# Optimization experiments

Hardware: AMD Instinct MI355X
Metric: run time of the kernel (lower is better)

## Reference

```python
import jax, jax.numpy as jnp
import numpy as np

D_MODEL = 1024
NUM_HEADS = 16
GROUP_SIZE = 4
NUM_GROUPS = NUM_HEADS // GROUP_SIZE  # 4
D_K = D_MODEL // NUM_HEADS            # 64
THETA = 10000.0
WINDOW = 512


def _rope(x, positions):
    # x: (..., t, d) with d even; interleaved-pair rotation, freq_i = theta^{-i/(d/2)}
    d = x.shape[-1]
    half = d // 2
    inv_freq = THETA ** (-jnp.arange(half, dtype=x.dtype) / half)          # (half,)
    ang = positions.astype(x.dtype)[:, None] * inv_freq[None, :]           # (t, half)
    cos, sin = jnp.cos(ang), jnp.sin(ang)
    x1, x2 = x[..., 0::2], x[..., 1::2]
    r1 = x1 * cos - x2 * sin
    r2 = x1 * sin + x2 * cos
    return jnp.stack([r1, r2], axis=-1).reshape(x.shape)


def setup_inputs() -> dict:
    key = jax.random.key(0)
    k1, k2, k3, k4, k5 = jax.random.split(key, 5)
    b, t = 2, 2048
    scale = 1.0 / np.sqrt(D_MODEL)
    return {
        "x": jax.random.normal(k1, (b, t, D_MODEL), dtype=jnp.float32),
        "WQ": jax.random.normal(k2, (D_MODEL, D_MODEL), dtype=jnp.float32) * scale,
        "WK": jax.random.normal(k3, (NUM_GROUPS * D_K, D_MODEL), dtype=jnp.float32) * scale,
        "WV": jax.random.normal(k4, (NUM_GROUPS * D_K, D_MODEL), dtype=jnp.float32) * scale,
        "WO": jax.random.normal(k5, (D_MODEL, D_MODEL), dtype=jnp.float32) * scale,
        "token_positions": jnp.arange(t, dtype=jnp.int32),
    }


def reference(x, WQ, WK, WV, WO, token_positions):
    b, t, _ = x.shape
    g, s, d = NUM_GROUPS, GROUP_SIZE, D_K
    # projections (Linear: y = x @ W^T, no bias)
    q = (x @ WQ.T).reshape(b, t, g, s, d).transpose(0, 2, 3, 1, 4)  # b g s t d
    k = (x @ WK.T).reshape(b, t, g, d).transpose(0, 2, 1, 3)        # b g t d
    v = (x @ WV.T).reshape(b, t, g, d).transpose(0, 2, 1, 3)        # b g t d
    q = _rope(q, token_positions)
    k = _rope(k, token_positions)
    # scores: kv heads shared across the s query heads of each group
    scores = jnp.einsum('bgsqd,bgkd->bgsqk', q, k) / jnp.sqrt(jnp.asarray(d, x.dtype))
    i = jnp.arange(t)[:, None]
    j = jnp.arange(t)[None, :]
    allowed = (i >= j) & (i - j <= WINDOW)  # causal sliding window
    scores = jnp.where(allowed, scores, -jnp.inf)
    probs = jax.nn.softmax(scores, axis=-1)
    out = jnp.einsum('bgsqk,bgkd->bgsqd', probs, v)                 # b g s t d
    out = out.transpose(0, 3, 1, 2, 4).reshape(b, t, D_MODEL)       # b t (g s d)
    return out @ WO.T
```

## Files before the change

### kernel.cpp

```cpp
#include <hip/hip_runtime.h>
#include <hip/hip_bf16.h>

typedef __bf16 bf16;
typedef __bf16 bf16x4 __attribute__((ext_vector_type(4)));
typedef __bf16 bf16x8 __attribute__((ext_vector_type(8)));
typedef float  floatx4 __attribute__((ext_vector_type(4)));

#define D_MODEL   1024
#define NUM_HEADS 16
#define NUM_GROUPS 4
#define DK        64
#define SEQ_T     2048
#define BATCH     2
#define M_ROWS    (BATCH*SEQ_T)
#define WINDOW    512
#define KV_DIM    (NUM_GROUPS*DK)
#define N_QKV     (D_MODEL + 2*KV_DIM)
#define QSCALE    0.1803368801111204f
#define FREQ_C    0.4152410118609203f

#define GLDS16(g, l)                                                          \
    __builtin_amdgcn_global_load_lds(                                         \
        (const __attribute__((address_space(1))) void*)(g),                   \
        (__attribute__((address_space(3))) void*)(l), 16, 0, 0)

__global__ __launch_bounds__(256)
void convert_all(const float* s0, bf16* d0, int c0,
                 const float* s1, bf16* d1, int c1,
                 const float* s2, bf16* d2, int c2,
                 const float* s3, bf16* d3, int c3,
                 const float* s4, bf16* d4, int c4)
{
    int id = blockIdx.x * 256 + threadIdx.x;
    const float* src; bf16* dst;
    if      (id < c0)         { src = s0; dst = d0; }
    else if ((id -= c0) < c1) { src = s1; dst = d1; }
    else if ((id -= c1) < c2) { src = s2; dst = d2; }
    else if ((id -= c2) < c3) { src = s3; dst = d3; }
    else if ((id -= c3) < c4) { src = s4; dst = d4; }
    else return;
    int i = id * 8;
    const float* s = src + i;
    float4 a = *(const float4*)s;
    float4 b = *(const float4*)(s + 4);
    bf16x8 v;
    v[0] = (bf16)a.x; v[1] = (bf16)a.y; v[2] = (bf16)a.z; v[3] = (bf16)a.w;
    v[4] = (bf16)b.x; v[5] = (bf16)b.y; v[6] = (bf16)b.z; v[7] = (bf16)b.w;
    *(bf16x8*)&dst[i] = v;
}

__global__ __launch_bounds__(256, 6)
void gemm_t64(const bf16* __restrict__ A, const bf16* __restrict__ W, int K,
              bf16* __restrict__ Cq, bf16* __restrict__ Ck, bf16* __restrict__ Vt,
              float* __restrict__ Co, const int* __restrict__ pos, int mode)
{
    __shared__ bf16 As0[64 * 32], As1[64 * 32];
    __shared__ bf16 Bs0[64 * 32], Bs1[64 * 32];

    const int tid  = threadIdx.x;
    const int wave = tid >> 6;
    const int lane = tid & 63;
    const int lr   = lane & 15;
    const int quad = lane >> 4;
    const int m0 = blockIdx.y * 64;
    const int n0 = blockIdx.x * 64;
    const int wm = (wave >> 1) * 32;
    const int wn = (wave & 1) * 32;

    const int srow = (lane >> 2);
    const int scol = (lane & 3) * 8;
    const bf16* Ap = &A[(size_t)(m0 + wave * 16 + srow) * K + scol];
    const bf16* Wp = &W[(size_t)(n0 + wave * 16 + srow) * K + scol];
    bf16* As0d = &As0[wave * 512];
    bf16* As1d = &As1[wave * 512];
    bf16* Bs0d = &Bs0[wave * 512];
    bf16* Bs1d = &Bs1[wave * 512];

    floatx4 acc[2][2];
#pragma unroll
    for (int i = 0; i < 2; i++)
#pragma unroll
        for (int j = 0; j < 2; j++) acc[i][j] = (floatx4)(0.0f);

    for (int k0 = 0; k0 < K; k0 += 64) {
        __syncthreads();
        GLDS16(Ap + k0,      As0d);
        GLDS16(Ap + k0 + 32, As1d);
        GLDS16(Wp + k0,      Bs0d);
        GLDS16(Wp + k0 + 32, Bs1d);
        __syncthreads();

        bf16x8 a0[2], a1[2], b0[2], b1[2];
#pragma unroll
        for (int mi = 0; mi < 2; mi++) {
            a0[mi] = *(const bf16x8*)&As0[(wm + mi * 16 + lr) * 32 + quad * 8];
            a1[mi] = *(const bf16x8*)&As1[(wm + mi * 16 + lr) * 32 + quad * 8];
        }
#pragma unroll
        for (int ni = 0; ni < 2; ni++) {
            b0[ni] = *(const bf16x8*)&Bs0[(wn + ni * 16 + lr) * 32 + quad * 8];
            b1[ni] = *(const bf16x8*)&Bs1[(wn + ni * 16 + lr) * 32 + quad * 8];
        }

#pragma unroll
        for (int mi = 0; mi < 2; mi++)
#pragma unroll
            for (int ni = 0; ni < 2; ni++) {
                acc[mi][ni] = __builtin_amdgcn_mfma_f32_16x16x32_bf16(
                    a0[mi], b0[ni], acc[mi][ni], 0, 0, 0);
                acc[mi][ni] = __builtin_amdgcn_mfma_f32_16x16x32_bf16(
                    a1[mi], b1[ni], acc[mi][ni], 0, 0, 0);
            }
    }

    if (mode == 0) {
        if (n0 >= D_MODEL + KV_DIM) {
            const int g  = (n0 - (D_MODEL + KV_DIM)) >> 6;
            const int b  = m0 >> 11;
            const int bg = b * 4 + g;
#pragma unroll
            for (int mi = 0; mi < 2; mi++) {
#pragma unroll
                for (int ni = 0; ni < 2; ni++) {
                    int d  = wn + ni * 16 + lr;
                    int t0 = (m0 & (SEQ_T - 1)) + wm + mi * 16 + quad * 4;
                    bf16x4 v;
#pragma unroll
                    for (int r = 0; r < 4; r++) v[r] = (bf16)acc[mi][ni][r];
                    *(bf16x4*)&Vt[((size_t)(bg * 64 + d)) * SEQ_T + t0] = v;
                }
            }
        } else {
            bf16* out; int ld, coff; float sc;
            if (n0 < D_MODEL) { out = Cq; ld = D_MODEL; coff = n0; sc = QSCALE; }
            else              { out = Ck; ld = KV_DIM;  coff = n0 - D_MODEL; sc = 1.0f; }
            float inv[2];
            float sgn = (lr & 1) ? 1.0f : -1.0f;
#pragma unroll
            for (int ni = 0; ni < 2; ni++) {
                int ip = (wn + ni * 16 + lr) >> 1;
                inv[ni] = exp2f(-(float)ip * FREQ_C);
            }
#pragma unroll
            for (int mi = 0; mi < 2; mi++) {
#pragma unroll
                for (int r = 0; r < 4; r++) {
                    int row = m0 + wm + mi * 16 + quad * 4 + r;
                    float p = (float)pos[row & (SEQ_T - 1)];
#pragma unroll
                    for (int ni = 0; ni < 2; ni++) {
                        float v  = acc[mi][ni][r];
                        float vp = __shfl_xor(v, 1);
                        float ang = p * inv[ni];
                        float ss, cc;
                        __sincosf(ang, &ss, &cc);
                        v = v * cc + vp * ss * sgn;
                        out[(size_t)row * ld + coff + wn + ni * 16 + lr] = (bf16)(v * sc);
                    }
                }
            }
        }
    } else {
#pragma unroll
        for (int mi = 0; mi < 2; mi++)
#pragma unroll
            for (int ni = 0; ni < 2; ni++)
#pragma unroll
                for (int r = 0; r < 4; r++) {
                    int row = m0 + wm + mi * 16 + quad * 4 + r;
                    int col = n0 + wn + ni * 16 + lr;
                    Co[(size_t)row * D_MODEL + col] = acc[mi][ni][r];
                }
    }
}

__global__ __launch_bounds__(256)
void attn_mfma(const bf16* __restrict__ Q, const bf16* __restrict__ K,
               const bf16* __restrict__ Vt_g, bf16* __restrict__ AO)
{
    const int ST = 72;
    __shared__ bf16 Ks[64 * ST];
    __shared__ bf16 Vt[80 * ST];
    __shared__ bf16 Ps[4 * 32 * ST];

    const int tid  = threadIdx.x;
    const int wave = tid >> 6;
    const int lane = tid & 63;
    const int lr   = lane & 15;
    const int quad = lane >> 4;
    const int bg = blockIdx.y;
    const int b = bg >> 2, g = bg & 3;
    const int h = g * 4 + wave;
    const int q0 = blockIdx.x * 32;

    bf16x8 qf[2][2];
#pragma unroll
    for (int mi = 0; mi < 2; mi++)
#pragma unroll
        for (int ks = 0; ks < 2; ks++)
            qf[mi][ks] = *(const bf16x8*)
                &Q[((size_t)(b * SEQ_T + q0 + mi * 16 + lr)) * D_MODEL
                   + h * 64 + ks * 32 + quad * 8];

    for (int i = tid; i < 15 * ST; i += 256) Vt[65 * ST + i] = (bf16)0.0f;
    if (tid < ST) Vt[64 * ST + tid] = (bf16)(tid < 64 ? 1.0f : 0.0f);

    bf16* Pw = &Ps[wave * 32 * ST];

    floatx4 o[2][5];
#pragma unroll
    for (int mi = 0; mi < 2; mi++)
#pragma unroll
        for (int nt = 0; nt < 5; nt++) o[mi][nt] = (floatx4)(0.0f);

    const int t0   = (q0 >= WINDOW) ? ((q0 - WINDOW) & ~63) : 0;
    const int last = q0 & ~63;

    for (int j0 = t0; j0 <= last; j0 += 64) {
        const bool mC = (j0 == last);
        const bool mW = (q0 >= WINDOW) && (j0 == t0);
        __syncthreads();
#pragma unroll
        for (int i = 0; i < 2; i++) {
            int c = tid + i * 256;
            int row = c >> 3, col8 = (c & 7) * 8;
            *(bf16x8*)&Ks[row * ST + col8] =
                *(const bf16x8*)&K[((size_t)(b * SEQ_T + j0 + row)) * KV_DIM + g * 64 + col8];
            *(bf16x8*)&Vt[row * ST + col8] =
                *(const bf16x8*)&Vt_g[((size_t)(bg * 64 + row)) * SEQ_T + j0 + col8];
        }
        __syncthreads();

        floatx4 s[2][4];
#pragma unroll
        for (int mi = 0; mi < 2; mi++)
#pragma unroll
            for (int nt = 0; nt < 4; nt++) s[mi][nt] = (floatx4)(0.0f);
#pragma unroll
        for (int ks = 0; ks < 2; ks++) {
#pragma unroll
            for (int nt = 0; nt < 4; nt++) {
                bf16x8 kf = *(const bf16x8*)&Ks[(nt * 16 + lr) * ST + ks * 32 + quad * 8];
                s[0][nt] = __builtin_amdgcn_mfma_f32_16x16x32_bf16(qf[0][ks], kf, s[0][nt], 0, 0, 0);
                s[1][nt] = __builtin_amdgcn_mfma_f32_16x16x32_bf16(qf[1][ks], kf, s[1][nt], 0, 0, 0);
            }
        }

        if (mC) {
#pragma unroll
            for (int mi = 0; mi < 2; mi++)
#pragma unroll
                for (int nt = 0; nt < 4; nt++) {
                    int key = j0 + nt * 16 + lr;
#pragma unroll
                    for (int r = 0; r < 4; r++) {
                        int qi_ = q0 + mi * 16 + quad * 4 + r;
                        s[mi][nt][r] = (key <= qi_) ? s[mi][nt][r] : -1e30f;
                    }
                }
        } else if (mW) {
#pragma unroll
            for (int mi = 0; mi < 2; mi++)
#pragma unroll
                for (int nt = 0; nt < 4; nt++) {
                    int key = j0 + nt * 16 + lr;
#pragma unroll
                    for (int r = 0; r < 4; r++) {
                        int qi_ = q0 + mi * 16 + quad * 4 + r;
                        s[mi][nt][r] = (qi_ - key <= WINDOW) ? s[mi][nt][r] : -1e30f;
                    }
                }
        }

#pragma unroll
        for (int mi = 0; mi < 2; mi++)
#pragma unroll
            for (int nt = 0; nt < 4; nt++)
#pragma unroll
                for (int r = 0; r < 4; r++)
                    Pw[(mi * 16 + quad * 4 + r) * ST + nt * 16 + lr] =
                        (bf16)exp2f(s[mi][nt][r]);

        __asm__ volatile("s_waitcnt lgkmcnt(0)" ::: "memory");

#pragma unroll
        for (int ks = 0; ks < 2; ks++) {
            bf16x8 pf0 = *(const bf16x8*)&Pw[(0 + lr) * ST + ks * 32 + quad * 8];
            bf16x8 pf1 = *(const bf16x8*)&Pw[(16 + lr) * ST + ks * 32 + quad * 8];
#pragma unroll
            for (int nt = 0; nt < 5; nt++) {
                bf16x8 vf = *(const bf16x8*)&Vt[(nt * 16 + lr) * ST + ks * 32 + quad * 8];
                o[0][nt] = __builtin_amdgcn_mfma_f32_16x16x32_bf16(pf0, vf, o[0][nt], 0, 0, 0);
                o[1][nt] = __builtin_amdgcn_mfma_f32_16x16x32_bf16(pf1, vf, o[1][nt], 0, 0, 0);
            }
        }
    }

#pragma unroll
    for (int mi = 0; mi < 2; mi++)
#pragma unroll
        for (int r = 0; r < 4; r++) {
            float l = __shfl(o[mi][4][r], lane & 48);
            float invl = 1.0f / l;
            int row = q0 + mi * 16 + quad * 4 + r;
#pragma unroll
            for (int nt = 0; nt < 4; nt++)
                AO[((size_t)(b * SEQ_T + row)) * D_MODEL + h * 64 + nt * 16 + lr] =
                    (bf16)(o[mi][nt][r] * invl);
        }
}

extern "C" void kernel_launch(void* const* d_in, const int* in_sizes, int n_in,
                              void* d_out, int out_size, void* d_ws, size_t ws_size,
                              hipStream_t stream)
{
    const float* x  = (const float*)d_in[0];
    const float* WQ = (const float*)d_in[1];
    const float* WK = (const float*)d_in[2];
    const float* WV = (const float*)d_in[3];
    const float* WO = (const float*)d_in[4];
    const int*  pos = (const int*)d_in[5];

    char* ws   = (char*)d_ws;
    bf16* Qw   = (bf16*)ws;
    bf16* Kw   = (bf16*)(ws + (size_t) 8 * 1024 * 1024);
    bf16* Vt_g = (bf16*)(ws + (size_t)10 * 1024 * 1024);
    bf16* xb   = (bf16*)(ws + (size_t)12 * 1024 * 1024);
    bf16* AO   = xb;
    bf16* Wqkv = (bf16*)(ws + (size_t)20 * 1024 * 1024);
    bf16* WOb  = (bf16*)(ws + (size_t)23 * 1024 * 1024);

    const int cx = (M_ROWS * D_MODEL) / 8;
    const int cq = (D_MODEL * D_MODEL) / 8;
    const int ck = (KV_DIM * D_MODEL) / 8;
    const int ctot = cx + cq + 2 * ck + cq;
    convert_all<<<ctot / 256, 256, 0, stream>>>(
        x, xb, cx,
        WQ, Wqkv, cq,
        WK, Wqkv + (size_t)D_MODEL * D_MODEL, ck,
        WV, Wqkv + (size_t)(D_MODEL + KV_DIM) * D_MODEL, ck,
        WO, WOb, cq);

    gemm_t64<<<dim3(N_QKV / 64, M_ROWS / 64), 256, 0, stream>>>(
        x ? xb : xb, Wqkv, D_MODEL, Qw, Kw, Vt_g, nullptr, pos, 0);

    attn_mfma<<<dim3(SEQ_T / 32, BATCH * NUM_GROUPS), 256, 0, stream>>>(
        Qw, Kw, Vt_g, AO);

    gemm_t64<<<dim3(D_MODEL / 64, M_ROWS / 64), 256, 0, stream>>>(
        AO, WOb, D_MODEL, nullptr, nullptr, nullptr, (float*)d_out, pos, 1);
}
```

Baseline: 150.1 us.

## Fuse all stages into one persistent kernel with grid-wide barriers

Replaces the four launches (convert, QKV GEMM, attention, output GEMM) with one persistent kernel of 512 blocks that runs each stage in turn and separates them with a software grid barrier built on atomics. Each block handles 3 QKV tiles, one attention tile and 2 output-projection tiles, and shared memory is reused across stages through a union. The aim is to remove launch gaps and tail effects between kernels. In exchange it depends on all 512 blocks being co-resident for the spin barrier, adds a memset, and lowers the launch-bounds occupancy hint to 3 blocks per CU, which could hurt latency hiding in the GEMMs.

Result: slower. 329.8 us (+119.8%).

```diff
diff --git a/kernel.cpp b/kernel.cpp
--- a/kernel.cpp
+++ b/kernel.cpp
@@ -18,76 +18,60 @@
 #define N_QKV     (D_MODEL + 2*KV_DIM)
 #define QSCALE    0.1803368801111204f
 #define FREQ_C    0.4152410118609203f
+#define GRID_B    512
 
 #define GLDS16(g, l)                                                          \
     __builtin_amdgcn_global_load_lds(                                         \
         (const __attribute__((address_space(1))) void*)(g),                   \
         (__attribute__((address_space(3))) void*)(l), 16, 0, 0)
 
-__global__ __launch_bounds__(256)
-void convert_all(const float* s0, bf16* d0, int c0,
-                 const float* s1, bf16* d1, int c1,
-                 const float* s2, bf16* d2, int c2,
-                 const float* s3, bf16* d3, int c3,
-                 const float* s4, bf16* d4, int c4)
+__device__ __forceinline__ void gbar(int* cnt, int* gen, int nb)
 {
-    int id = blockIdx.x * 256 + threadIdx.x;
-    const float* src; bf16* dst;
-    if      (id < c0)         { src = s0; dst = d0; }
-    else if ((id -= c0) < c1) { src = s1; dst = d1; }
-    else if ((id -= c1) < c2) { src = s2; dst = d2; }
-    else if ((id -= c2) < c3) { src = s3; dst = d3; }
-    else if ((id -= c3) < c4) { src = s4; dst = d4; }
-    else return;
-    int i = id * 8;
-    const float* s = src + i;
-    float4 a = *(const float4*)s;
-    float4 b = *(const float4*)(s + 4);
-    bf16x8 v;
-    v[0] = (bf16)a.x; v[1] = (bf16)a.y; v[2] = (bf16)a.z; v[3] = (bf16)a.w;
-    v[4] = (bf16)b.x; v[5] = (bf16)b.y; v[6] = (bf16)b.z; v[7] = (bf16)b.w;
-    *(bf16x8*)&dst[i] = v;
+    __syncthreads();
+    if (threadIdx.x == 0) {
+        __threadfence();
+        int g = atomicAdd(gen, 0);
+        int a = atomicAdd(cnt, 1);
+        if (a == nb - 1) {
+            atomicSub(cnt, nb);
+            __threadfence();
+            atomicAdd(gen, 1);
+        } else {
+            while (atomicAdd(gen, 0) == g) __builtin_amdgcn_s_sleep(2);
+        }
+        __threadfence();
+    }
+    __syncthreads();
 }
 
-__global__ __launch_bounds__(256, 6)
-void gemm_t64(const bf16* __restrict__ A, const bf16* __restrict__ W, int K,
-              bf16* __restrict__ Cq, bf16* __restrict__ Ck, bf16* __restrict__ Vt,
-              float* __restrict__ Co, const int* __restrict__ pos, int mode)
+__device__ __forceinline__
+void gemm_body(const bf16* __restrict__ A, const bf16* __restrict__ W,
+               bf16* As0, bf16* As1, bf16* Bs0, bf16* Bs1,
+               int m0, int n0, floatx4 acc[2][2])
 {
-    __shared__ bf16 As0[64 * 32], As1[64 * 32];
-    __shared__ bf16 Bs0[64 * 32], Bs1[64 * 32];
-
     const int tid  = threadIdx.x;
     const int wave = tid >> 6;
     const int lane = tid & 63;
     const int lr   = lane & 15;
     const int quad = lane >> 4;
-    const int m0 = blockIdx.y * 64;
-    const int n0 = blockIdx.x * 64;
     const int wm = (wave >> 1) * 32;
     const int wn = (wave & 1) * 32;
-
     const int srow = (lane >> 2);
     const int scol = (lane & 3) * 8;
-    const bf16* Ap = &A[(size_t)(m0 + wave * 16 + srow) * K + scol];
-    const bf16* Wp = &W[(size_t)(n0 + wave * 16 + srow) * K + scol];
-    bf16* As0d = &As0[wave * 512];
-    bf16* As1d = &As1[wave * 512];
-    bf16* Bs0d = &Bs0[wave * 512];
-    bf16* Bs1d = &Bs1[wave * 512];
-
-    floatx4 acc[2][2];
+    const bf16* Ap = &A[(size_t)(m0 + wave * 16 + srow) * 1024 + scol];
+    const bf16* Wp = &W[(size_t)(n0 + wave * 16 + srow) * 1024 + scol];
+
 #pragma unroll
     for (int i = 0; i < 2; i++)
 #pragma unroll
         for (int j = 0; j < 2; j++) acc[i][j] = (floatx4)(0.0f);
 
-    for (int k0 = 0; k0 < K; k0 += 64) {
+    for (int k0 = 0; k0 < 1024; k0 += 64) {
         __syncthreads();
-        GLDS16(Ap + k0,      As0d);
-        GLDS16(Ap + k0 + 32, As1d);
-        GLDS16(Wp + k0,      Bs0d);
-        GLDS16(Wp + k0 + 32, Bs1d);
+        GLDS16(Ap + k0,      As0 + wave * 512);
+        GLDS16(Ap + k0 + 32, As1 + wave * 512);
+        GLDS16(Wp + k0,      Bs0 + wave * 512);
+        GLDS16(Wp + k0 + 32, Bs1 + wave * 512);
         __syncthreads();
 
         bf16x8 a0[2], a1[2], b0[2], b1[2];
@@ -101,7 +85,6 @@
             b0[ni] = *(const bf16x8*)&Bs0[(wn + ni * 16 + lr) * 32 + quad * 8];
             b1[ni] = *(const bf16x8*)&Bs1[(wn + ni * 16 + lr) * 32 + quad * 8];
         }
-
 #pragma unroll
         for (int mi = 0; mi < 2; mi++)
 #pragma unroll
@@ -112,14 +95,70 @@
                     a1[mi], b1[ni], acc[mi][ni], 0, 0, 0);
             }
     }
-
-    if (mode == 0) {
+}
+
+__global__ __launch_bounds__(256, 3)
+void fused_all(const float* __restrict__ x,   const float* __restrict__ WQf,
+               const float* __restrict__ WKf, const float* __restrict__ WVf,
+               const float* __restrict__ WOf, const int* __restrict__ pos,
+               bf16* __restrict__ xb,  bf16* __restrict__ Wqkv,
+               bf16* __restrict__ WOb, bf16* __restrict__ Qw,
+               bf16* __restrict__ Kw,  bf16* __restrict__ Vt_g,
+               bf16* __restrict__ AO,  float* __restrict__ out,
+               int* __restrict__ bar)
+{
+    __shared__ union {
+        struct { bf16 As0[2048], As1[2048], Bs0[2048], Bs1[2048]; } g;
+        struct { bf16 Ks[64 * 72], Vt[80 * 72], Ps[4 * 32 * 72]; } a;
+    } u;
+
+    const int tid  = threadIdx.x;
+    const int wave = tid >> 6;
+    const int lane = tid & 63;
+    const int lr   = lane & 15;
+    const int quad = lane >> 4;
+
+    {
+        const int cx = (M_ROWS * D_MODEL) / 8;
+        const int cq = (D_MODEL * D_MODEL) / 8;
+        const int ck = (KV_DIM * D_MODEL) / 8;
+        const int total = cx + cq + 2 * ck + cq;
+        for (int id0 = blockIdx.x * 256 + tid; id0 < total; id0 += GRID_B * 256) {
+            int id = id0;
+            const float* src; bf16* dst;
+            if      (id < cx)         { src = x;   dst = xb; }
+            else if ((id -= cx) < cq) { src = WQf; dst = Wqkv; }
+            else if ((id -= cq) < ck) { src = WKf; dst = Wqkv + (size_t)D_MODEL * D_MODEL; }
+            else if ((id -= ck) < ck) { src = WVf; dst = Wqkv + (size_t)(D_MODEL + KV_DIM) * D_MODEL; }
+            else                      { id -= ck;  src = WOf; dst = WOb; }
+            int i = id * 8;
+            const float* s = src + i;
+            float4 a = *(const float4*)s;
+            float4 b = *(const float4*)(s + 4);
+            bf16x8 v;
+            v[0] = (bf16)a.x; v[1] = (bf16)a.y; v[2] = (bf16)a.z; v[3] = (bf16)a.w;
+            v[4] = (bf16)b.x; v[5] = (bf16)b.y; v[6] = (bf16)b.z; v[7] = (bf16)b.w;
+            *(bf16x8*)&dst[i] = v;
+        }
+    }
+    gbar(&bar[0], &bar[1], GRID_B);
+
+#pragma unroll 1
+    for (int it = 0; it < 3; it++) {
+        int t  = blockIdx.x * 3 + it;
+        int n0 = (t % 24) * 64;
+        int m0 = (t / 24) * 64;
+        floatx4 acc[2][2];
+        gemm_body(xb, Wqkv, u.g.As0, u.g.As1, u.g.Bs0, u.g.Bs1, m0, n0, acc);
+
+        const int wm = (wave >> 1) * 32;
+        const int wn = (wave & 1) * 32;
         if (n0 >= D_MODEL + KV_DIM) {
             const int g  = (n0 - (D_MODEL + KV_DIM)) >> 6;
             const int b  = m0 >> 11;
             const int bg = b * 4 + g;
 #pragma unroll
-            for (int mi = 0; mi < 2; mi++) {
+            for (int mi = 0; mi < 2; mi++)
 #pragma unroll
                 for (int ni = 0; ni < 2; ni++) {
                     int d  = wn + ni * 16 + lr;
@@ -127,13 +166,12 @@
                     bf16x4 v;
 #pragma unroll
                     for (int r = 0; r < 4; r++) v[r] = (bf16)acc[mi][ni][r];
-                    *(bf16x4*)&Vt[((size_t)(bg * 64 + d)) * SEQ_T + t0] = v;
-                }
-            }
+                    *(bf16x4*)&Vt_g[((size_t)(bg * 64 + d)) * SEQ_T + t0] = v;
+                }
         } else {
-            bf16* out; int ld, coff; float sc;
-            if (n0 < D_MODEL) { out = Cq; ld = D_MODEL; coff = n0; sc = QSCALE; }
-            else              { out = Ck; ld = KV_DIM;  coff = n0 - D_MODEL; sc = 1.0f; }
+            bf16* o_; int ld, coff; float sc;
+            if (n0 < D_MODEL) { o_ = Qw; ld = D_MODEL; coff = n0; sc = QSCALE; }
+            else              { o_ = Kw; ld = KV_DIM;  coff = n0 - D_MODEL; sc = 1.0f; }
             float inv[2];
             float sgn = (lr & 1) ? 1.0f : -1.0f;
 #pragma unroll
@@ -142,7 +180,7 @@
                 inv[ni] = exp2f(-(float)ip * FREQ_C);
             }
 #pragma unroll
-            for (int mi = 0; mi < 2; mi++) {
+            for (int mi = 0; mi < 2; mi++)
 #pragma unroll
                 for (int r = 0; r < 4; r++) {
                     int row = m0 + wm + mi * 16 + quad * 4 + r;
@@ -155,12 +193,150 @@
                         float ss, cc;
                         __sincosf(ang, &ss, &cc);
                         v = v * cc + vp * ss * sgn;
-                        out[(size_t)row * ld + coff + wn + ni * 16 + lr] = (bf16)(v * sc);
+                        o_[(size_t)row * ld + coff + wn + ni * 16 + lr] = (bf16)(v * sc);
                     }
                 }
-            }
-        }
-    } else {
+        }
+    }
+    gbar(&bar[0], &bar[1], GRID_B);
+
+    {
+        const int ST = 72;
+        bf16* Ks = u.a.Ks;
+        bf16* Vt = u.a.Vt;
+        bf16* Pw = &u.a.Ps[wave * 32 * ST];
+
+        const int bg = blockIdx.x >> 6;
+        const int b = bg >> 2, g = bg & 3;
+        const int h = g * 4 + wave;
+        const int q0 = (blockIdx.x & 63) * 32;
+
+        bf16x8 qf[2][2];
+#pragma unroll
+        for (int mi = 0; mi < 2; mi++)
+#pragma unroll
+            for (int ks = 0; ks < 2; ks++)
+                qf[mi][ks] = *(const bf16x8*)
+                    &Qw[((size_t)(b * SEQ_T + q0 + mi * 16 + lr)) * D_MODEL
+                        + h * 64 + ks * 32 + quad * 8];
+
+        for (int i = tid; i < 15 * ST; i += 256) Vt[65 * ST + i] = (bf16)0.0f;
+        if (tid < ST) Vt[64 * ST + tid] = (bf16)(tid < 64 ? 1.0f : 0.0f);
+
+        floatx4 o[2][5];
+#pragma unroll
+        for (int mi = 0; mi < 2; mi++)
+#pragma unroll
+            for (int nt = 0; nt < 5; nt++) o[mi][nt] = (floatx4)(0.0f);
+
+        const int t0   = (q0 >= WINDOW) ? ((q0 - WINDOW) & ~63) : 0;
+        const int last = q0 & ~63;
+
+        for (int j0 = t0; j0 <= last; j0 += 64) {
+            const bool mC = (j0 == last);
+            const bool mW = (q0 >= WINDOW) && (j0 == t0);
+            __syncthreads();
+#pragma unroll
+            for (int i = 0; i < 2; i++) {
+                int c = tid + i * 256;
+                int row = c >> 3, col8 = (c & 7) * 8;
+                *(bf16x8*)&Ks[row * ST + col8] =
+                    *(const bf16x8*)&Kw[((size_t)(b * SEQ_T + j0 + row)) * KV_DIM + g * 64 + col8];
+                *(bf16x8*)&Vt[row * ST + col8] =
+                    *(const bf16x8*)&Vt_g[((size_t)(bg * 64 + row)) * SEQ_T + j0 + col8];
+            }
+            __syncthreads();
+
+            floatx4 s[2][4];
+#pragma unroll
+            for (int mi = 0; mi < 2; mi++)
+#pragma unroll
+                for (int nt = 0; nt < 4; nt++) s[mi][nt] = (floatx4)(0.0f);
+#pragma unroll
+            for (int ks = 0; ks < 2; ks++) {
+#pragma unroll
+                for (int nt = 0; nt < 4; nt++) {
+                    bf16x8 kf = *(const bf16x8*)&Ks[(nt * 16 + lr) * ST + ks * 32 + quad * 8];
+                    s[0][nt] = __builtin_amdgcn_mfma_f32_16x16x32_bf16(qf[0][ks], kf, s[0][nt], 0, 0, 0);
+                    s[1][nt] = __builtin_amdgcn_mfma_f32_16x16x32_bf16(qf[1][ks], kf, s[1][nt], 0, 0, 0);
+                }
+            }
+
+            if (mC) {
+#pragma unroll
+                for (int mi = 0; mi < 2; mi++)
+#pragma unroll
+                    for (int nt = 0; nt < 4; nt++) {
+                        int key = j0 + nt * 16 + lr;
+#pragma unroll
+                        for (int r = 0; r < 4; r++) {
+                            int qi_ = q0 + mi * 16 + quad * 4 + r;
+                            s[mi][nt][r] = (key <= qi_) ? s[mi][nt][r] : -1e30f;
+                        }
+                    }
+            } else if (mW) {
+#pragma unroll
+                for (int mi = 0; mi < 2; mi++)
+#pragma unroll
+                    for (int nt = 0; nt < 4; nt++) {
+                        int key = j0 + nt * 16 + lr;
+#pragma unroll
+                        for (int r = 0; r < 4; r++) {
+                            int qi_ = q0 + mi * 16 + quad * 4 + r;
+                            s[mi][nt][r] = (qi_ - key <= WINDOW) ? s[mi][nt][r] : -1e30f;
+                        }
+                    }
+            }
+
+#pragma unroll
+            for (int mi = 0; mi < 2; mi++)
+#pragma unroll
+                for (int nt = 0; nt < 4; nt++)
+#pragma unroll
+                    for (int r = 0; r < 4; r++)
+                        Pw[(mi * 16 + quad * 4 + r) * ST + nt * 16 + lr] =
+                            (bf16)exp2f(s[mi][nt][r]);
+
+            __asm__ volatile("s_waitcnt lgkmcnt(0)" ::: "memory");
+
+#pragma unroll
+            for (int ks = 0; ks < 2; ks++) {
+                bf16x8 pf0 = *(const bf16x8*)&Pw[(0 + lr) * ST + ks * 32 + quad * 8];
+                bf16x8 pf1 = *(const bf16x8*)&Pw[(16 + lr) * ST + ks * 32 + quad * 8];
+#pragma unroll
+                for (int nt = 0; nt < 5; nt++) {
+                    bf16x8 vf = *(const bf16x8*)&Vt[(nt * 16 + lr) * ST + ks * 32 + quad * 8];
+                    o[0][nt] = __builtin_amdgcn_mfma_f32_16x16x32_bf16(pf0, vf, o[0][nt], 0, 0, 0);
+                    o[1][nt] = __builtin_amdgcn_mfma_f32_16x16x32_bf16(pf1, vf, o[1][nt], 0, 0, 0);
+                }
+            }
+        }
+
+#pragma unroll
+        for (int mi = 0; mi < 2; mi++)
+#pragma unroll
+            for (int r = 0; r < 4; r++) {
+                float l = __shfl(o[mi][4][r], lane & 48);
+                float invl = 1.0f / l;
+                int row = q0 + mi * 16 + quad * 4 + r;
+#pragma unroll
+                for (int nt = 0; nt < 4; nt++)
+                    AO[((size_t)(b * SEQ_T + row)) * D_MODEL + h * 64 + nt * 16 + lr] =
+                        (bf16)(o[mi][nt][r] * invl);
+            }
+    }
+    gbar(&bar[0], &bar[1], GRID_B);
+
+#pragma unroll 1
+    for (int it = 0; it < 2; it++) {
+        int t  = blockIdx.x * 2 + it;
+        int n0 = (t % 16) * 64;
+        int m0 = (t / 16) * 64;
+        floatx4 acc[2][2];
+        gemm_body(AO, WOb, u.g.As0, u.g.As1, u.g.Bs0, u.g.Bs1, m0, n0, acc);
+
+        const int wm = (wave >> 1) * 32;
+        const int wn = (wave & 1) * 32;
 #pragma unroll
         for (int mi = 0; mi < 2; mi++)
 #pragma unroll
@@ -169,145 +345,9 @@
                 for (int r = 0; r < 4; r++) {
                     int row = m0 + wm + mi * 16 + quad * 4 + r;
                     int col = n0 + wn + ni * 16 + lr;
-                    Co[(size_t)row * D_MODEL + col] = acc[mi][ni][r];
-                }
-    }
-}
-
-__global__ __launch_bounds__(256)
-void attn_mfma(const bf16* __restrict__ Q, const bf16* __restrict__ K,
-               const bf16* __restrict__ Vt_g, bf16* __restrict__ AO)
-{
-    const int ST = 72;
-    __shared__ bf16 Ks[64 * ST];
-    __shared__ bf16 Vt[80 * ST];
-    __shared__ bf16 Ps[4 * 32 * ST];
-
-    const int tid  = threadIdx.x;
-    const int wave = tid >> 6;
-    const int lane = tid & 63;
-    const int lr   = lane & 15;
-    const int quad = lane >> 4;
-    const int bg = blockIdx.y;
-    const int b = bg >> 2, g = bg & 3;
-    const int h = g * 4 + wave;
-    const int q0 = blockIdx.x * 32;
-
-    bf16x8 qf[2][2];
-#pragma unroll
-    for (int mi = 0; mi < 2; mi++)
-#pragma unroll
-        for (int ks = 0; ks < 2; ks++)
-            qf[mi][ks] = *(const bf16x8*)
-                &Q[((size_t)(b * SEQ_T + q0 + mi * 16 + lr)) * D_MODEL
-                   + h * 64 + ks * 32 + quad * 8];
-
-    for (int i = tid; i < 15 * ST; i += 256) Vt[65 * ST + i] = (bf16)0.0f;
-    if (tid < ST) Vt[64 * ST + tid] = (bf16)(tid < 64 ? 1.0f : 0.0f);
-
-    bf16* Pw = &Ps[wave * 32 * ST];
-
-    floatx4 o[2][5];
-#pragma unroll
-    for (int mi = 0; mi < 2; mi++)
-#pragma unroll
-        for (int nt = 0; nt < 5; nt++) o[mi][nt] = (floatx4)(0.0f);
-
-    const int t0   = (q0 >= WINDOW) ? ((q0 - WINDOW) & ~63) : 0;
-    const int last = q0 & ~63;
-
-    for (int j0 = t0; j0 <= last; j0 += 64) {
-        const bool mC = (j0 == last);
-        const bool mW = (q0 >= WINDOW) && (j0 == t0);
-        __syncthreads();
-#pragma unroll
-        for (int i = 0; i < 2; i++) {
-            int c = tid + i * 256;
-            int row = c >> 3, col8 = (c & 7) * 8;
-            *(bf16x8*)&Ks[row * ST + col8] =
-                *(const bf16x8*)&K[((size_t)(b * SEQ_T + j0 + row)) * KV_DIM + g * 64 + col8];
-            *(bf16x8*)&Vt[row * ST + col8] =
-                *(const bf16x8*)&Vt_g[((size_t)(bg * 64 + row)) * SEQ_T + j0 + col8];
-        }
-        __syncthreads();
-
-        floatx4 s[2][4];
-#pragma unroll
-        for (int mi = 0; mi < 2; mi++)
-#pragma unroll
-            for (int nt = 0; nt < 4; nt++) s[mi][nt] = (floatx4)(0.0f);
-#pragma unroll
-        for (int ks = 0; ks < 2; ks++) {
-#pragma unroll
-            for (int nt = 0; nt < 4; nt++) {
-                bf16x8 kf = *(const bf16x8*)&Ks[(nt * 16 + lr) * ST + ks * 32 + quad * 8];
-                s[0][nt] = __builtin_amdgcn_mfma_f32_16x16x32_bf16(qf[0][ks], kf, s[0][nt], 0, 0, 0);
-                s[1][nt] = __builtin_amdgcn_mfma_f32_16x16x32_bf16(qf[1][ks], kf, s[1][nt], 0, 0, 0);
-            }
-        }
-
-        if (mC) {
-#pragma unroll
-            for (int mi = 0; mi < 2; mi++)
-#pragma unroll
-                for (int nt = 0; nt < 4; nt++) {
-                    int key = j0 + nt * 16 + lr;
-#pragma unroll
-                    for (int r = 0; r < 4; r++) {
-                        int qi_ = q0 + mi * 16 + quad * 4 + r;
-                        s[mi][nt][r] = (key <= qi_) ? s[mi][nt][r] : -1e30f;
-                    }
-                }
-        } else if (mW) {
-#pragma unroll
-            for (int mi = 0; mi < 2; mi++)
-#pragma unroll
-                for (int nt = 0; nt < 4; nt++) {
-                    int key = j0 + nt * 16 + lr;
-#pragma unroll
-                    for (int r = 0; r < 4; r++) {
-                        int qi_ = q0 + mi * 16 + quad * 4 + r;
-                        s[mi][nt][r] = (qi_ - key <= WINDOW) ? s[mi][nt][r] : -1e30f;
-                    }
-                }
-        }
-
-#pragma unroll
-        for (int mi = 0; mi < 2; mi++)
-#pragma unroll
-            for (int nt = 0; nt < 4; nt++)
-#pragma unroll
-                for (int r = 0; r < 4; r++)
-                    Pw[(mi * 16 + quad * 4 + r) * ST + nt * 16 + lr] =
-                        (bf16)exp2f(s[mi][nt][r]);
-
-        __asm__ volatile("s_waitcnt lgkmcnt(0)" ::: "memory");
-
-#pragma unroll
-        for (int ks = 0; ks < 2; ks++) {
-            bf16x8 pf0 = *(const bf16x8*)&Pw[(0 + lr) * ST + ks * 32 + quad * 8];
-            bf16x8 pf1 = *(const bf16x8*)&Pw[(16 + lr) * ST + ks * 32 + quad * 8];
-#pragma unroll
-            for (int nt = 0; nt < 5; nt++) {
-                bf16x8 vf = *(const bf16x8*)&Vt[(nt * 16 + lr) * ST + ks * 32 + quad * 8];
-                o[0][nt] = __builtin_amdgcn_mfma_f32_16x16x32_bf16(pf0, vf, o[0][nt], 0, 0, 0);
-                o[1][nt] = __builtin_amdgcn_mfma_f32_16x16x32_bf16(pf1, vf, o[1][nt], 0, 0, 0);
-            }
-        }
-    }
-
-#pragma unroll
-    for (int mi = 0; mi < 2; mi++)
-#pragma unroll
-        for (int r = 0; r < 4; r++) {
-            float l = __shfl(o[mi][4][r], lane & 48);
-            float invl = 1.0f / l;
-            int row = q0 + mi * 16 + quad * 4 + r;
-#pragma unroll
-            for (int nt = 0; nt < 4; nt++)
-                AO[((size_t)(b * SEQ_T + row)) * D_MODEL + h * 64 + nt * 16 + lr] =
-                    (bf16)(o[mi][nt][r] * invl);
-        }
+                    out[(size_t)row * D_MODEL + col] = acc[mi][ni][r];
+                }
+    }
 }
 
 extern "C" void kernel_launch(void* const* d_in, const int* in_sizes, int n_in,
@@ -320,6 +360,7 @@
     const float* WV = (const float*)d_in[3];
     const float* WO = (const float*)d_in[4];
     const int*  pos = (const int*)d_in[5];
+    float* outp = (float*)d_out;
 
     char* ws   = (char*)d_ws;
     bf16* Qw   = (bf16*)ws;
@@ -329,24 +370,9 @@
     bf16* AO   = xb;
     bf16* Wqkv = (bf16*)(ws + (size_t)20 * 1024 * 1024);
     bf16* WOb  = (bf16*)(ws + (size_t)23 * 1024 * 1024);
-
-    const int cx = (M_ROWS * D_MODEL) / 8;
-    const int cq = (D_MODEL * D_MODEL) / 8;
-    const int ck = (KV_DIM * D_MODEL) / 8;
-    const int ctot = cx + cq + 2 * ck + cq;
-    convert_all<<<ctot / 256, 256, 0, stream>>>(
-        x, xb, cx,
-        WQ, Wqkv, cq,
-        WK, Wqkv + (size_t)D_MODEL * D_MODEL, ck,
-        WV, Wqkv + (size_t)(D_MODEL + KV_DIM) * D_MODEL, ck,
-        WO, WOb, cq);
-
-    gemm_t64<<<dim3(N_QKV / 64, M_ROWS / 64), 256, 0, stream>>>(
-        x ? xb : xb, Wqkv, D_MODEL, Qw, Kw, Vt_g, nullptr, pos, 0);
-
-    attn_mfma<<<dim3(SEQ_T / 32, BATCH * NUM_GROUPS), 256, 0, stream>>>(
-        Qw, Kw, Vt_g, AO);
-
-    gemm_t64<<<dim3(D_MODEL / 64, M_ROWS / 64), 256, 0, stream>>>(
-        AO, WOb, D_MODEL, nullptr, nullptr, nullptr, (float*)d_out, pos, 1);
+    int*  bar  = (int*)(ws + (size_t)26 * 1024 * 1024);
+
+    hipMemsetAsync(bar, 0, 256, stream);
+    fused_all<<<GRID_B, 256, 0, stream>>>(
+        x, WQ, WK, WV, WO, pos, xb, Wqkv, WOb, Qw, Kw, Vt_g, AO, outp, bar);
 }
```
